# Kernel optimization log

Measured on AMD Instinct MI355X. Metric: run time of the kernel, lower is better.

The kernel has to match this reference:

```python
import jax, jax.numpy as jnp
import numpy as np

NUM_ENVS = 16384
NUM_AGENTS = 16
IN_DIM = 128
GCN_H = 64
RNN_H = 64
E_PER_GRAPH = 128
N_FEAT = 4   # num_individual_actions_features
N_CAT = 8    # num_action_categories
OUT_DIM = NUM_AGENTS * N_FEAT * N_CAT


def setup_inputs() -> dict:
    key = jax.random.key(0)
    ks = jax.random.split(key, 10)
    x = jax.random.normal(ks[0], (NUM_ENVS, NUM_AGENTS, IN_DIM), dtype=jnp.float32)
    edge_index = jax.random.randint(ks[1], (NUM_ENVS, 2, E_PER_GRAPH), 0, NUM_AGENTS, dtype=jnp.int64)
    prev_h = jax.random.normal(ks[2], (NUM_ENVS, NUM_AGENTS, RNN_H), dtype=jnp.float32)
    s = 0.05
    W_gcn = jax.random.normal(ks[3], (IN_DIM, GCN_H), dtype=jnp.float32) * s
    b_gcn = jnp.zeros((GCN_H,), dtype=jnp.float32)
    W_ih = jax.random.normal(ks[4], (3 * RNN_H, GCN_H), dtype=jnp.float32) * s
    W_hh = jax.random.normal(ks[5], (3 * RNN_H, RNN_H), dtype=jnp.float32) * s
    b_ih = jax.random.normal(ks[6], (3 * RNN_H,), dtype=jnp.float32) * s
    b_hh = jax.random.normal(ks[7], (3 * RNN_H,), dtype=jnp.float32) * s
    W_lin = jax.random.normal(ks[8], (OUT_DIM, NUM_AGENTS * RNN_H), dtype=jnp.float32) * s
    b_lin = jax.random.normal(ks[9], (OUT_DIM,), dtype=jnp.float32) * s
    return {"x": x, "edge_index": edge_index, "prev_rnn_hidden_state": prev_h,
            "W_gcn": W_gcn, "b_gcn": b_gcn, "W_ih": W_ih, "W_hh": W_hh,
            "b_ih": b_ih, "b_hh": b_hh, "W_lin": W_lin, "b_lin": b_lin}


def _forward(x, edge_index, prev_h, W_gcn, b_gcn, W_ih, W_hh, b_ih, b_hh, W_lin, b_lin):
    num_envs = x.shape[0]
    N = num_envs * NUM_AGENTS  # flattened node count
    x_flat = x.reshape(N, IN_DIM)

    # block-offset trick: one big disconnected graph
    offsets = (jnp.arange(num_envs, dtype=edge_index.dtype) * NUM_AGENTS)[:, None, None]  # [env,1,1]
    ei = (edge_index + offsets).reshape(num_envs, 2, -1)  # offsets broadcast over [env,2,E]
    row = ei[:, 0, :].reshape(-1)  # source nodes, [env*E]
    col = ei[:, 1, :].reshape(-1)  # target nodes

    # GCNConv: xw = x @ W; add self-loops; sym-normalize; scatter-add to targets
    xw = x_flat @ W_gcn  # [N, GCN_H]
    ones_e = jnp.ones(row.shape[0], dtype=x.dtype)
    deg = jnp.ones((N,), dtype=x.dtype) + jax.ops.segment_sum(ones_e, col, num_segments=N)
    dinv = jax.lax.rsqrt(deg)
    norm = dinv[row] * dinv[col]  # [env*E]
    msg = norm[:, None] * xw[row]  # gather + scale
    agg = jnp.zeros_like(xw).at[col].add(msg)
    agg = agg + xw / deg[:, None]  # self-loop term: 1/deg * xw
    gcn_out = agg + b_gcn  # [N, GCN_H]

    # single-step GRU (torch gate order: r, z, n)
    h = prev_h.reshape(N, RNN_H)
    gx = gcn_out @ W_ih.T + b_ih  # [N, 3H]
    gh = h @ W_hh.T + b_hh
    rx, zx, nx = jnp.split(gx, 3, axis=-1)
    rh, zh, nh = jnp.split(gh, 3, axis=-1)
    r = jax.nn.sigmoid(rx + rh)
    z = jax.nn.sigmoid(zx + zh)
    n = jnp.tanh(nx + r * nh)
    h_new = (1.0 - z) * n + z * h  # [N, H]

    flat = h_new.reshape(num_envs, NUM_AGENTS * RNN_H)
    logits = flat @ W_lin.T + b_lin  # [env, OUT_DIM]
    next_h = h_new.reshape(num_envs, NUM_AGENTS, RNN_H)
    return logits, next_h


def reference(x, edge_index, prev_rnn_hidden_state, W_gcn, b_gcn, W_ih, W_hh, b_ih, b_hh, W_lin, b_lin):
    return _forward(x, edge_index, prev_rnn_hidden_state, W_gcn, b_gcn, W_ih, W_hh, b_ih, b_hh, W_lin, b_lin)
```

## Files before the change

### kernel.cpp

```cpp
#include <hip/hip_runtime.h>
#include <math.h>

namespace {

constexpr int NUM_ENVS = 16384;
constexpr int OUT_DIM = 512;
constexpr int FLAT = 1024;

typedef float floatx4 __attribute__((ext_vector_type(4)));
typedef short shortx8 __attribute__((ext_vector_type(8)));

__device__ __forceinline__ float fast_sigmoid(float v) {
    const float e = __builtin_amdgcn_exp2f(-v * 1.44269504088896340736f);
    return __builtin_amdgcn_rcpf(1.0f + e);
}
__device__ __forceinline__ float fast_tanh(float v) {
    const float e = __builtin_amdgcn_exp2f(v * 2.88539008177792681472f);
    return 1.0f - 2.0f * __builtin_amdgcn_rcpf(1.0f + e);
}
__device__ __forceinline__ unsigned short f2bf(float f) {
    unsigned int u = __float_as_uint(f);
    u = (u + 0x7FFFu + ((u >> 16) & 1u)) >> 16;
    return (unsigned short)u;
}
__device__ __forceinline__ shortx8 pack8(const float4& f0, const float4& f1) {
    shortx8 o;
    o[0] = (short)f2bf(f0.x); o[1] = (short)f2bf(f0.y);
    o[2] = (short)f2bf(f0.z); o[3] = (short)f2bf(f0.w);
    o[4] = (short)f2bf(f1.x); o[5] = (short)f2bf(f1.y);
    o[6] = (short)f2bf(f1.z); o[7] = (short)f2bf(f1.w);
    return o;
}

constexpr int WS_FLAG = 0;
constexpr int WS_WGF  = 64;
constexpr int WS_WCF  = WS_WGF + 4096;
constexpr int WS_WLB  = WS_WCF + 12288;
constexpr int WS_GB   = WS_WLB + 262144;

__global__ void prep_kernel(const int* __restrict__ edges_i32,
                            const float* __restrict__ Wg,
                            const float* __restrict__ Wih,
                            const float* __restrict__ Whh,
                            const float* __restrict__ Wlin,
                            float* __restrict__ ws) {
    if (blockIdx.x == 0) {
        __shared__ int any_nonzero;
        if (threadIdx.x == 0) any_nonzero = 0;
        __syncthreads();
        if (threadIdx.x < 128 && edges_i32[2 * threadIdx.x + 1] != 0)
            atomicOr(&any_nonzero, 1);
        __syncthreads();
        if (threadIdx.x == 0) ((int*)ws)[WS_FLAG] = (any_nonzero == 0) ? 1 : 0;
        return;
    }
    const int t = ((int)blockIdx.x - 1) * 256 + (int)threadIdx.x;
    if (t < 8192) {
        const int jj = t & 7, lane = (t >> 3) & 63, slot = t >> 9;
        const int nt = slot >> 2, ks = slot & 3;
        const int n = nt * 16 + (lane & 15);
        const int k = ks * 32 + ((lane >> 4) & 3) * 8 + jj;
        ((unsigned short*)(ws + WS_WGF))[t] = f2bf(Wg[k * 64 + n]);
    } else if (t < 32768) {
        const int u = t - 8192;
        const int jj = u & 7, lane = (u >> 3) & 63, slot = u >> 9;
        const int q8 = ((lane >> 4) & 3) * 8 + jj;
        float val;
        if (slot < 16) {
            const int nt = slot >> 2, ks = slot & 3;
            const int n = nt * 16 + (lane & 15);
            const int k = ks * 32 + q8;
            val = (k < 64) ? Wih[n * 64 + k] : Whh[n * 64 + (k - 64)];
        } else if (slot < 32) {
            const int s = slot - 16, nt = s >> 2, ks = s & 3;
            const int n = 64 + nt * 16 + (lane & 15);
            const int k = ks * 32 + q8;
            val = (k < 64) ? Wih[n * 64 + k] : Whh[n * 64 + (k - 64)];
        } else if (slot < 40) {
            const int s = slot - 32, nt = s >> 1, ks = s & 1;
            const int n = 128 + nt * 16 + (lane & 15);
            val = Wih[n * 64 + ks * 32 + q8];
        } else {
            const int s = slot - 40, nt = s >> 1, ks = s & 1;
            const int n = 128 + nt * 16 + (lane & 15);
            val = Whh[n * 64 + ks * 32 + q8];
        }
        ((unsigned short*)(ws + WS_WCF))[u] = f2bf(val);
    } else if (t < 32768 + 524288) {
        const int u = t - 32768;
        ((unsigned short*)(ws + WS_WLB))[u] = f2bf(Wlin[u]);
    }
}

__global__ __launch_bounds__(256, 4) void fused_gcn_gru_kernel(
    const float* __restrict__ x,
    const void*  __restrict__ edges,
    const unsigned short* __restrict__ WgF,
    const float* __restrict__ bg,
    const float* __restrict__ h_prev,
    const unsigned short* __restrict__ WcF,
    const float* __restrict__ bih,
    const float* __restrict__ bhh,
    float* __restrict__ next_h,
    unsigned short* __restrict__ hb,
    const int* __restrict__ flag64)
{
    const int b = blockIdx.x;
    const int tid = threadIdx.x;
    const int lane = tid & 63;
    const int w = tid >> 6;

    __shared__ float xw_s[64 * 68];
    __shared__ unsigned short A_s[64 * 72];
    __shared__ int rc_s[512];
    __shared__ float adj_s[4][16][17];
    __shared__ int deg_s[4][16];
    __shared__ float dinv_s[4][16];
    __shared__ float invdeg_s[4][16];

    const int ar = w * 16 + (lane & 15);
    const int aq = (lane >> 4) & 3;

    float4 xf[4][2];
    #pragma unroll
    for (int ks = 0; ks < 4; ++ks) {
        const float4* p = (const float4*)(x + ((size_t)b * 64 + ar) * 128 + ks * 32 + aq * 8);
        xf[ks][0] = p[0];
        xf[ks][1] = p[1];
    }
    shortx8 hfr2, hfr3;
    {
        const float* hp4 = h_prev + ((size_t)b * 64 + ar) * 64;
        const float4* pa = (const float4*)(hp4 + aq * 8);
        hfr2 = pack8(pa[0], pa[1]);
        const float4* pb = (const float4*)(hp4 + 32 + aq * 8);
        hfr3 = pack8(pb[0], pb[1]);
    }

    {
        float* ap = &adj_s[0][0][0];
        for (int i = tid; i < 4 * 16 * 17; i += 256) ap[i] = 0.0f;
        if (tid < 64) deg_s[tid >> 4][tid & 15] = 0;
    }
    const bool is64 = (*flag64 != 0);
    #pragma unroll
    for (int t = 0; t < 2; ++t) {
        const int e = tid + 256 * t;
        const int el = e >> 7, idx = e & 127;
        const size_t base = ((size_t)b * 4 + el) * 256;
        int rv, cv;
        if (is64) {
            rv = (int)((const long long*)edges)[base + idx];
            cv = (int)((const long long*)edges)[base + 128 + idx];
        } else {
            rv = ((const int*)edges)[base + idx];
            cv = ((const int*)edges)[base + 128 + idx];
        }
        rc_s[e] = rv | (cv << 8);
    }
    __syncthreads();

    #pragma unroll
    for (int t = 0; t < 2; ++t) {
        const int e = tid + 256 * t;
        atomicAdd(&deg_s[e >> 7][(rc_s[e] >> 8) & 15], 1);
    }

    shortx8 afr[4];
    #pragma unroll
    for (int ks = 0; ks < 4; ++ks) afr[ks] = pack8(xf[ks][0], xf[ks][1]);
    floatx4 acc[4];
    #pragma unroll
    for (int nt = 0; nt < 4; ++nt) acc[nt] = (floatx4)(0.0f);
    #pragma unroll
    for (int nt = 0; nt < 4; ++nt) {
        #pragma unroll
        for (int ks = 0; ks < 4; ++ks) {
            const shortx8 bfr = *(const shortx8*)&WgF[((nt * 4 + ks) * 64 + lane) * 8];
            acc[nt] = __builtin_amdgcn_mfma_f32_16x16x32_bf16(afr[ks], bfr, acc[nt], 0, 0, 0);
        }
    }
    __syncthreads();

    if (tid < 64) {
        const float d = 1.0f + (float)deg_s[tid >> 4][tid & 15];
        dinv_s[tid >> 4][tid & 15] = rsqrtf(d);
        invdeg_s[tid >> 4][tid & 15] = 1.0f / d;
    }
    #pragma unroll
    for (int nt = 0; nt < 4; ++nt)
        #pragma unroll
        for (int i = 0; i < 4; ++i)
            xw_s[(w * 16 + aq * 4 + i) * 68 + nt * 16 + (lane & 15)] = acc[nt][i];
    __syncthreads();

    #pragma unroll
    for (int t = 0; t < 2; ++t) {
        const int e = tid + 256 * t;
        const int el = e >> 7;
        const int r = rc_s[e] & 15, c = (rc_s[e] >> 8) & 15;
        atomicAdd(&adj_s[el][c][r], dinv_s[el][r] * dinv_s[el][c]);
    }
    if (tid < 64)
        atomicAdd(&adj_s[tid >> 4][tid & 15][tid & 15], invdeg_s[tid >> 4][tid & 15]);
    __syncthreads();

    {
        const int ro = tid >> 2, q = tid & 3;
        const int el = ro >> 4, cl = ro & 15;
        float accs[16];
        #pragma unroll
        for (int m = 0; m < 16; ++m) accs[m] = 0.0f;
        for (int r16 = 0; r16 < 16; ++r16) {
            const float a = adj_s[el][cl][r16];
            const float4* xr = (const float4*)&xw_s[(el * 16 + r16) * 68 + q * 16];
            #pragma unroll
            for (int jq = 0; jq < 4; ++jq) {
                const float4 v = xr[jq];
                accs[4 * jq + 0] += a * v.x;
                accs[4 * jq + 1] += a * v.y;
                accs[4 * jq + 2] += a * v.z;
                accs[4 * jq + 3] += a * v.w;
            }
        }
        unsigned short* dst = &A_s[ro * 72 + q * 16];
        shortx8 o0, o1;
        #pragma unroll
        for (int m = 0; m < 8; ++m) o0[m] = (short)f2bf(accs[m] + bg[q * 16 + m]);
        #pragma unroll
        for (int m = 0; m < 8; ++m) o1[m] = (short)f2bf(accs[8 + m] + bg[q * 16 + 8 + m]);
        *(shortx8*)dst = o0;
        *(shortx8*)(dst + 8) = o1;
    }
    __syncthreads();

    shortx8 gfr[4];
    gfr[0] = *(const shortx8*)&A_s[ar * 72 + aq * 8];
    gfr[1] = *(const shortx8*)&A_s[ar * 72 + 32 + aq * 8];
    gfr[2] = hfr2;
    gfr[3] = hfr3;
    floatx4 aR[4], aZ[4], aNX[4], aNH[4];
    #pragma unroll
    for (int nt = 0; nt < 4; ++nt) {
        aR[nt] = (floatx4)(0.0f); aZ[nt] = (floatx4)(0.0f);
        aNX[nt] = (floatx4)(0.0f); aNH[nt] = (floatx4)(0.0f);
    }
    #pragma unroll
    for (int nt = 0; nt < 4; ++nt) {
        #pragma unroll
        for (int ks = 0; ks < 4; ++ks) {
            const shortx8 bfr = *(const shortx8*)&WcF[((nt * 4 + ks) * 64 + lane) * 8];
            aR[nt] = __builtin_amdgcn_mfma_f32_16x16x32_bf16(gfr[ks], bfr, aR[nt], 0, 0, 0);
        }
        #pragma unroll
        for (int ks = 0; ks < 4; ++ks) {
            const shortx8 bfr = *(const shortx8*)&WcF[((16 + nt * 4 + ks) * 64 + lane) * 8];
            aZ[nt] = __builtin_amdgcn_mfma_f32_16x16x32_bf16(gfr[ks], bfr, aZ[nt], 0, 0, 0);
        }
        #pragma unroll
        for (int ks = 0; ks < 2; ++ks) {
            const shortx8 bfr = *(const shortx8*)&WcF[((32 + nt * 2 + ks) * 64 + lane) * 8];
            aNX[nt] = __builtin_amdgcn_mfma_f32_16x16x32_bf16(gfr[ks], bfr, aNX[nt], 0, 0, 0);
        }
        #pragma unroll
        for (int ks = 0; ks < 2; ++ks) {
            const shortx8 bfr = *(const shortx8*)&WcF[((40 + nt * 2 + ks) * 64 + lane) * 8];
            aNH[nt] = __builtin_amdgcn_mfma_f32_16x16x32_bf16(gfr[ks + 2], bfr, aNH[nt], 0, 0, 0);
        }
    }

    const int cl2 = lane & 15;
    const int rq = (lane >> 4) & 3;
    #pragma unroll
    for (int tp = 0; tp < 4; ++tp) {
        const int f = tp * 16 + cl2;
        const float br = bih[f] + bhh[f];
        const float bz = bih[64 + f] + bhh[64 + f];
        const float bnx = bih[128 + f];
        const float bnh = bhh[128 + f];
        #pragma unroll
        for (int i = 0; i < 4; ++i) {
            const int rl = w * 16 + rq * 4 + i;
            const size_t row = (size_t)b * 64 + rl;
            const float hp = h_prev[row * 64 + f];
            const float r = fast_sigmoid(aR[tp][i] + br);
            const float z = fast_sigmoid(aZ[tp][i] + bz);
            const float n = fast_tanh(aNX[tp][i] + bnx + r * (aNH[tp][i] + bnh));
            const float hv = (1.0f - z) * n + z * hp;
            next_h[row * 64 + f] = hv;
            hb[row * 64 + f] = f2bf(hv);
        }
    }
}

__global__ __launch_bounds__(256, 2) void logits_mfma_kernel(
    const unsigned short* __restrict__ A,
    const unsigned short* __restrict__ B,
    const float* __restrict__ bias,
    float* __restrict__ C)
{
    __shared__ __align__(16) unsigned short As[2][128 * 64];
    __shared__ __align__(16) unsigned short Bs[2][128 * 64];

    const int tid = threadIdx.x;
    const int lane = tid & 63;
    const int wave = tid >> 6;
    const int wr = wave >> 1;
    const int wc = wave & 1;
    const int m0 = blockIdx.y * 128;
    const int n0 = blockIdx.x * 128;
    const int lr = tid >> 3;
    const int lk = tid & 7;

    floatx4 acc[4][4];
    #pragma unroll
    for (int i = 0; i < 4; ++i)
        #pragma unroll
        for (int jn = 0; jn < 4; ++jn)
            acc[i][jn] = (floatx4)(0.0f);

    uint4 ra[4], rb[4];
    auto load_tile = [&](int kt) {
        const int k0 = kt * 64;
        #pragma unroll
        for (int i = 0; i < 4; ++i) {
            const int r = lr + 32 * i;
            ra[i] = *(const uint4*)&A[(size_t)(m0 + r) * FLAT + k0 + lk * 8];
            rb[i] = *(const uint4*)&B[(size_t)(n0 + r) * FLAT + k0 + lk * 8];
        }
    };
    auto write_tile = [&](int buf) {
        #pragma unroll
        for (int i = 0; i < 4; ++i) {
            const int r = lr + 32 * i;
            *(uint4*)&As[buf][r * 64 + ((lk ^ (r & 7)) * 8)] = ra[i];
            *(uint4*)&Bs[buf][r * 64 + ((lk ^ (r & 7)) * 8)] = rb[i];
        }
    };

    load_tile(0);
    write_tile(0);
    __syncthreads();

    #pragma unroll 2
    for (int kt = 0; kt < 16; ++kt) {
        const int cur = kt & 1;
        if (kt < 15) load_tile(kt + 1);
        #pragma unroll
        for (int s = 0; s < 2; ++s) {
            const int kg = s * 4 + (lane >> 4);
            const int sw = (kg ^ (lane & 7)) * 8;
            shortx8 af[4], bf[4];
            #pragma unroll
            for (int t = 0; t < 4; ++t) {
                af[t] = *(const shortx8*)&As[cur][(wr * 64 + t * 16 + (lane & 15)) * 64 + sw];
                bf[t] = *(const shortx8*)&Bs[cur][(wc * 64 + t * 16 + (lane & 15)) * 64 + sw];
            }
            #pragma unroll
            for (int mt = 0; mt < 4; ++mt)
                #pragma unroll
                for (int nt = 0; nt < 4; ++nt)
                    acc[mt][nt] = __builtin_amdgcn_mfma_f32_16x16x32_bf16(
                        af[mt], bf[nt], acc[mt][nt], 0, 0, 0);
        }
        if (kt < 15) {
            write_tile(cur ^ 1);
            __syncthreads();
        }
    }

    const int col_l = lane & 15;
    const int rg = lane >> 4;
    #pragma unroll
    for (int nt = 0; nt < 4; ++nt) {
        const int col = n0 + wc * 64 + nt * 16 + col_l;
        const float bv = bias[col];
        #pragma unroll
        for (int mt = 0; mt < 4; ++mt) {
            const int row = m0 + wr * 64 + mt * 16 + rg * 4;
            #pragma unroll
            for (int i = 0; i < 4; ++i) {
                C[(size_t)(row + i) * OUT_DIM + col] = acc[mt][nt][i] + bv;
            }
        }
    }
}

}

extern "C" void kernel_launch(void* const* d_in, const int* in_sizes, int n_in,
                              void* d_out, int out_size, void* d_ws, size_t ws_size,
                              hipStream_t stream) {
    const float* x    = (const float*)d_in[0];
    const void*  ei   = d_in[1];
    const float* h0   = (const float*)d_in[2];
    const float* Wg   = (const float*)d_in[3];
    const float* bg   = (const float*)d_in[4];
    const float* Wih  = (const float*)d_in[5];
    const float* Whh  = (const float*)d_in[6];
    const float* bih  = (const float*)d_in[7];
    const float* bhh  = (const float*)d_in[8];
    const float* Wlin = (const float*)d_in[9];
    const float* blin = (const float*)d_in[10];

    float* out = (float*)d_out;
    float* logits = out;
    float* next_h = out + (size_t)NUM_ENVS * OUT_DIM;

    float* wsf = (float*)d_ws;
    int* flag = (int*)(wsf + WS_FLAG);
    unsigned short* WgF = (unsigned short*)(wsf + WS_WGF);
    unsigned short* WcF = (unsigned short*)(wsf + WS_WCF);
    unsigned short* Wlb = (unsigned short*)(wsf + WS_WLB);
    unsigned short* gb  = (unsigned short*)(wsf + WS_GB);

    prep_kernel<<<2177, 256, 0, stream>>>((const int*)ei, Wg, Wih, Whh, Wlin, wsf);
    fused_gcn_gru_kernel<<<4096, 256, 0, stream>>>(x, ei, WgF, bg, h0, WcF, bih, bhh,
                                                   next_h, gb, flag);
    dim3 g2(OUT_DIM / 128, NUM_ENVS / 128);
    logits_mfma_kernel<<<g2, 256, 0, stream>>>(gb, Wlb, blin, logits);
}
```

Measured before the change: 388.2 us.

## Make each wave own one environment and replace block barriers with wave fences

Restructures the fused GCN+GRU kernel so that each wavefront handles a single environment end to end. All shared-memory staging (edges, adjacency, degrees, xw, GCN output) becomes per-wave, which lets every __syncthreads be replaced by an lgkmcnt wait. The previous hidden state is loaded once with coalesced float4 reads, stored as bf16 into shared memory, and reused both as the MFMA operand and for the GRU blend, so h_prev is no longer reloaded from global memory. The risk is that the blend now uses a bf16-rounded h_prev instead of fp32, which loses some accuracy. The design also relies on the lockstep execution of a wave for correctness of its shared-memory writes.

```diff
diff --git a/kernel.cpp b/kernel.cpp
--- a/kernel.cpp
+++ b/kernel.cpp
@@ -9,6 +9,8 @@
 
 typedef float floatx4 __attribute__((ext_vector_type(4)));
 typedef short shortx8 __attribute__((ext_vector_type(8)));
+
+#define WAVE_FENCE() asm volatile("s_waitcnt lgkmcnt(0)" ::: "memory")
 
 __device__ __forceinline__ float fast_sigmoid(float v) {
     const float e = __builtin_amdgcn_exp2f(-v * 1.44269504088896340736f);
@@ -22,6 +24,9 @@
     unsigned int u = __float_as_uint(f);
     u = (u + 0x7FFFu + ((u >> 16) & 1u)) >> 16;
     return (unsigned short)u;
+}
+__device__ __forceinline__ float bf2f(unsigned short s) {
+    return __uint_as_float(((unsigned int)s) << 16);
 }
 __device__ __forceinline__ shortx8 pack8(const float4& f0, const float4& f1) {
     shortx8 o;
@@ -109,62 +114,66 @@
     const int tid = threadIdx.x;
     const int lane = tid & 63;
     const int w = tid >> 6;
-
-    __shared__ float xw_s[64 * 68];
-    __shared__ unsigned short A_s[64 * 72];
-    __shared__ int rc_s[512];
+    const int env = b * 4 + w;
+
+    __shared__ float xw_s[4][16 * 68];
+    __shared__ unsigned short A_s[4][16 * 136];
     __shared__ float adj_s[4][16][17];
-    __shared__ int deg_s[4][16];
+    __shared__ int   deg_s[4][16];
     __shared__ float dinv_s[4][16];
     __shared__ float invdeg_s[4][16];
 
-    const int ar = w * 16 + (lane & 15);
-    const int aq = (lane >> 4) & 3;
+    const int ar = lane & 15;
+    const int aq = lane >> 4;
 
     float4 xf[4][2];
     #pragma unroll
     for (int ks = 0; ks < 4; ++ks) {
-        const float4* p = (const float4*)(x + ((size_t)b * 64 + ar) * 128 + ks * 32 + aq * 8);
+        const float4* p = (const float4*)(x + ((size_t)env * 16 + ar) * 128 + ks * 32 + aq * 8);
         xf[ks][0] = p[0];
         xf[ks][1] = p[1];
     }
-    shortx8 hfr2, hfr3;
+    float4 hf[4];
     {
-        const float* hp4 = h_prev + ((size_t)b * 64 + ar) * 64;
-        const float4* pa = (const float4*)(hp4 + aq * 8);
-        hfr2 = pack8(pa[0], pa[1]);
-        const float4* pb = (const float4*)(hp4 + 32 + aq * 8);
-        hfr3 = pack8(pb[0], pb[1]);
+        const float4* src = (const float4*)(h_prev + ((size_t)env * 16 + ar) * 64 + aq * 16);
+        hf[0] = src[0]; hf[1] = src[1]; hf[2] = src[2]; hf[3] = src[3];
+    }
+    const bool is64 = (*flag64 != 0);
+    int rv[2], cv[2];
+    const size_t ebase = (size_t)env * 256;
+    #pragma unroll
+    for (int t = 0; t < 2; ++t) {
+        const int idx = lane + 64 * t;
+        long long rvl, cvl;
+        if (is64) {
+            rvl = ((const long long*)edges)[ebase + idx];
+            cvl = ((const long long*)edges)[ebase + 128 + idx];
+        } else {
+            rvl = ((const int*)edges)[ebase + idx];
+            cvl = ((const int*)edges)[ebase + 128 + idx];
+        }
+        rv[t] = (int)rvl & 15;
+        cv[t] = (int)cvl & 15;
     }
 
     {
-        float* ap = &adj_s[0][0][0];
-        for (int i = tid; i < 4 * 16 * 17; i += 256) ap[i] = 0.0f;
-        if (tid < 64) deg_s[tid >> 4][tid & 15] = 0;
-    }
-    const bool is64 = (*flag64 != 0);
-    #pragma unroll
-    for (int t = 0; t < 2; ++t) {
-        const int e = tid + 256 * t;
-        const int el = e >> 7, idx = e & 127;
-        const size_t base = ((size_t)b * 4 + el) * 256;
-        int rv, cv;
-        if (is64) {
-            rv = (int)((const long long*)edges)[base + idx];
-            cv = (int)((const long long*)edges)[base + 128 + idx];
-        } else {
-            rv = ((const int*)edges)[base + idx];
-            cv = ((const int*)edges)[base + 128 + idx];
-        }
-        rc_s[e] = rv | (cv << 8);
-    }
-    __syncthreads();
-
-    #pragma unroll
-    for (int t = 0; t < 2; ++t) {
-        const int e = tid + 256 * t;
-        atomicAdd(&deg_s[e >> 7][(rc_s[e] >> 8) & 15], 1);
-    }
+        float* ap = &adj_s[w][0][0];
+        #pragma unroll
+        for (int i = 0; i < 5; ++i) {
+            const int j = lane + 64 * i;
+            if (j < 272) ap[j] = 0.0f;
+        }
+        if (lane < 16) deg_s[w][lane] = 0;
+    }
+    {
+        unsigned short* dp = &A_s[w][ar * 136 + 64 + aq * 16];
+        *(shortx8*)dp = pack8(hf[0], hf[1]);
+        *(shortx8*)(dp + 8) = pack8(hf[2], hf[3]);
+    }
+    WAVE_FENCE();
+
+    #pragma unroll
+    for (int t = 0; t < 2; ++t) atomicAdd(&deg_s[w][cv[t]], 1);
 
     shortx8 afr[4];
     #pragma unroll
@@ -180,40 +189,35 @@
             acc[nt] = __builtin_amdgcn_mfma_f32_16x16x32_bf16(afr[ks], bfr, acc[nt], 0, 0, 0);
         }
     }
-    __syncthreads();
-
-    if (tid < 64) {
-        const float d = 1.0f + (float)deg_s[tid >> 4][tid & 15];
-        dinv_s[tid >> 4][tid & 15] = rsqrtf(d);
-        invdeg_s[tid >> 4][tid & 15] = 1.0f / d;
+    WAVE_FENCE();
+
+    if (lane < 16) {
+        const float d = 1.0f + (float)deg_s[w][lane];
+        dinv_s[w][lane] = rsqrtf(d);
+        invdeg_s[w][lane] = 1.0f / d;
     }
     #pragma unroll
     for (int nt = 0; nt < 4; ++nt)
         #pragma unroll
         for (int i = 0; i < 4; ++i)
-            xw_s[(w * 16 + aq * 4 + i) * 68 + nt * 16 + (lane & 15)] = acc[nt][i];
-    __syncthreads();
-
-    #pragma unroll
-    for (int t = 0; t < 2; ++t) {
-        const int e = tid + 256 * t;
-        const int el = e >> 7;
-        const int r = rc_s[e] & 15, c = (rc_s[e] >> 8) & 15;
-        atomicAdd(&adj_s[el][c][r], dinv_s[el][r] * dinv_s[el][c]);
-    }
-    if (tid < 64)
-        atomicAdd(&adj_s[tid >> 4][tid & 15][tid & 15], invdeg_s[tid >> 4][tid & 15]);
-    __syncthreads();
+            xw_s[w][(aq * 4 + i) * 68 + nt * 16 + ar] = acc[nt][i];
+    WAVE_FENCE();
+
+    #pragma unroll
+    for (int t = 0; t < 2; ++t)
+        atomicAdd(&adj_s[w][cv[t]][rv[t]], dinv_s[w][rv[t]] * dinv_s[w][cv[t]]);
+    if (lane < 16)
+        atomicAdd(&adj_s[w][lane][lane], invdeg_s[w][lane]);
+    WAVE_FENCE();
 
     {
-        const int ro = tid >> 2, q = tid & 3;
-        const int el = ro >> 4, cl = ro & 15;
+        const int cl = lane >> 2, q = lane & 3;
         float accs[16];
         #pragma unroll
         for (int m = 0; m < 16; ++m) accs[m] = 0.0f;
         for (int r16 = 0; r16 < 16; ++r16) {
-            const float a = adj_s[el][cl][r16];
-            const float4* xr = (const float4*)&xw_s[(el * 16 + r16) * 68 + q * 16];
+            const float a = adj_s[w][cl][r16];
+            const float4* xr = (const float4*)&xw_s[w][r16 * 68 + q * 16];
             #pragma unroll
             for (int jq = 0; jq < 4; ++jq) {
                 const float4 v = xr[jq];
@@ -223,7 +227,7 @@
                 accs[4 * jq + 3] += a * v.w;
             }
         }
-        unsigned short* dst = &A_s[ro * 72 + q * 16];
+        unsigned short* dst = &A_s[w][cl * 136 + q * 16];
         shortx8 o0, o1;
         #pragma unroll
         for (int m = 0; m < 8; ++m) o0[m] = (short)f2bf(accs[m] + bg[q * 16 + m]);
@@ -232,13 +236,13 @@
         *(shortx8*)dst = o0;
         *(shortx8*)(dst + 8) = o1;
     }
-    __syncthreads();
+    WAVE_FENCE();
 
     shortx8 gfr[4];
-    gfr[0] = *(const shortx8*)&A_s[ar * 72 + aq * 8];
-    gfr[1] = *(const shortx8*)&A_s[ar * 72 + 32 + aq * 8];
-    gfr[2] = hfr2;
-    gfr[3] = hfr3;
+    gfr[0] = *(const shortx8*)&A_s[w][ar * 136 + aq * 8];
+    gfr[1] = *(const shortx8*)&A_s[w][ar * 136 + 32 + aq * 8];
+    gfr[2] = *(const shortx8*)&A_s[w][ar * 136 + 64 + aq * 8];
+    gfr[3] = *(const shortx8*)&A_s[w][ar * 136 + 96 + aq * 8];
     floatx4 aR[4], aZ[4], aNX[4], aNH[4];
     #pragma unroll
     for (int nt = 0; nt < 4; ++nt) {
@@ -270,7 +274,7 @@
     }
 
     const int cl2 = lane & 15;
-    const int rq = (lane >> 4) & 3;
+    const int rq = lane >> 4;
     #pragma unroll
     for (int tp = 0; tp < 4; ++tp) {
         const int f = tp * 16 + cl2;
@@ -280,9 +284,9 @@
         const float bnh = bhh[128 + f];
         #pragma unroll
         for (int i = 0; i < 4; ++i) {
-            const int rl = w * 16 + rq * 4 + i;
-            const size_t row = (size_t)b * 64 + rl;
-            const float hp = h_prev[row * 64 + f];
+            const int rl = rq * 4 + i;
+            const size_t row = (size_t)env * 16 + rl;
+            const float hp = bf2f(A_s[w][rl * 136 + 64 + f]);
             const float r = fast_sigmoid(aR[tp][i] + br);
             const float z = fast_sigmoid(aZ[tp][i] + bz);
             const float n = fast_tanh(aNX[tp][i] + bnx + r * (aNH[tp][i] + bnh));
```

Measured after the change: 395.1 us. About the same (+1.8%).
